# Optimization experiments

Measured on AMD Instinct MI355X. Metric: run time of the kernel, lower is better.

## Reference

```python
import jax, jax.numpy as jnp
import numpy as np

H = 32        # num_attention_heads
KVH = 8       # num_key_value_heads
D = 64        # head_dim
HID = 2048    # hidden_size
G = H // KVH  # num_key_value_groups


def setup_inputs() -> dict:
    key = jax.random.key(0)
    k1, k2, k3, k4, k5 = jax.random.split(key, 5)
    B, S = 1, 2048
    s = 1.0 / np.sqrt(HID)
    return {
        "hidden_states": jax.random.normal(k1, (B, S, HID), dtype=jnp.float32),
        "attention_mask": jnp.ones((B, S), dtype=jnp.int32),
        "Wq": jax.random.normal(k2, (H * D, HID), dtype=jnp.float32) * s,
        "Wk": jax.random.normal(k3, (KVH * D, HID), dtype=jnp.float32) * s,
        "Wv": jax.random.normal(k4, (KVH * D, HID), dtype=jnp.float32) * s,
        "Wo": jax.random.normal(k5, (HID, HID), dtype=jnp.float32) * s,
    }


def reference(hidden_states, attention_mask, Wq, Wk, Wv, Wo):
    B, S, _ = hidden_states.shape
    dtype = hidden_states.dtype

    q = (hidden_states @ Wq.T).reshape(B, S, H, D).transpose(0, 2, 1, 3)     # [B,H,S,D]
    k = (hidden_states @ Wk.T).reshape(B, S, KVH, D).transpose(0, 2, 1, 3)   # [B,KVH,S,D]
    v = (hidden_states @ Wv.T).reshape(B, S, KVH, D).transpose(0, 2, 1, 3)

    # repeat_interleave over head dim: each KV head serves G query heads
    k = jnp.repeat(k, G, axis=1)  # [B,H,S,D]
    v = jnp.repeat(v, G, axis=1)

    scores = jnp.einsum('bhqd,bhkd->bhqk', q, k) / np.sqrt(D)  # [B,H,S,S]

    causal = jnp.tril(jnp.ones((S, S), dtype=dtype))                # [S,S]
    am = attention_mask.astype(dtype)[:, None, None, :]              # [B,1,1,S]
    mask = am * causal[None, None, :, :]                             # [B,1,S,S]
    mask = (1.0 - mask) * jnp.finfo(dtype).min
    scores = scores + mask                                           # broadcast over heads

    weights = jax.nn.softmax(scores, axis=-1)
    attn = jnp.einsum('bhqk,bhkd->bhqd', weights, v)                 # [B,H,S,D]
    attn = attn.transpose(0, 2, 1, 3).reshape(B, S, HID)
    return attn @ Wo.T
```

## Files before the change

### kernel.cpp

```cpp
#include <hip/hip_runtime.h>
#include <hip/hip_bf16.h>
#include <math.h>

typedef __attribute__((ext_vector_type(4))) float f32x4;
typedef __attribute__((ext_vector_type(16))) float f32x16;
typedef __attribute__((ext_vector_type(8))) short bf16x8;
typedef __attribute__((ext_vector_type(4))) short s16x4;
typedef __attribute__((ext_vector_type(4))) unsigned int u32x4;
typedef __attribute__((ext_vector_type(2))) unsigned int u32x2;
typedef short s16;
typedef unsigned int u32;
typedef unsigned short u16;

#define S_LEN 2048
#define HIDN  2048
#define QKVW  3072
#define NH    32
#define NKVH  8
#define HD    64

__device__ __forceinline__ s16 f2bf(float f) {
  unsigned int u = __float_as_uint(f);
  unsigned int lsb = (u >> 16) & 1u;
  u += 0x7fffu + lsb;
  return (s16)(u >> 16);
}

__device__ __forceinline__ u32 cvtpk(float lo, float hi) {
  u32 r;
  asm("v_cvt_pk_bf16_f32 %0, %1, %2" : "=v"(r) : "v"(lo), "v"(hi));
  return r;
}

__device__ __forceinline__ void gload16(const void* g, void* l) {
  __builtin_amdgcn_global_load_lds(
      (const __attribute__((address_space(1))) void*)g,
      (__attribute__((address_space(3))) void*)l, 16, 0, 0);
}

__device__ __forceinline__ void pls(u32& a, u32& b) {
  asm volatile("v_permlane32_swap_b32 %0, %1" : "+v"(a), "+v"(b));
}

__device__ __forceinline__ int swz7(int row) { return (row ^ (row >> 3)) & 7; }

__global__ __launch_bounds__(256) void cvt_all(const float* __restrict__ h,
                                               const float* __restrict__ wq,
                                               const float* __restrict__ wk,
                                               const float* __restrict__ wv,
                                               const float* __restrict__ wo,
                                               s16x4* __restrict__ dst) {
  int i = blockIdx.x * 256 + threadIdx.x;
  const float* src; int off;
  if (i < 1048576)      { src = h;  off = i; }
  else if (i < 2097152) { src = wq; off = i - 1048576; }
  else if (i < 2359296) { src = wk; off = i - 2097152; }
  else if (i < 2621440) { src = wv; off = i - 2359296; }
  else                  { src = wo; off = i - 2621440; }
  if (i < 3670016) {
    float4 f = reinterpret_cast<const float4*>(src)[off];
    s16x4 o;
    o.x = f2bf(f.x); o.y = f2bf(f.y); o.z = f2bf(f.z); o.w = f2bf(f.w);
    dst[i] = o;
  }
}

__device__ __forceinline__ void storeC(s16* C, size_t idx, float v)   { C[idx] = f2bf(v); }
__device__ __forceinline__ void storeC(float* C, size_t idx, float v) { C[idx] = v; }

template <typename OUT_T>
__global__ __launch_bounds__(512) void gemm_bt(const s16* __restrict__ A,
                                               const s16* __restrict__ B,
                                               OUT_T* __restrict__ C,
                                               int M, int N, int K) {
  __shared__ alignas(16) s16 As[2][8192];
  __shared__ alignas(16) s16 Bs[2][8192];

  const int t    = threadIdx.x;
  const int lane = t & 63;
  const int w    = t >> 6;
  const int wr   = (w >> 2) * 64;
  const int wc   = (w & 3) * 32;
  const int lr   = lane & 15;
  const int lg   = lane >> 4;
  const int bm   = blockIdx.y * 128;
  const int bn   = blockIdx.x * 128;

  const int srow0 = (w * 2) * 8 + (lane >> 3);
  const int srow1 = (w * 2 + 1) * 8 + (lane >> 3);
  const int sl0   = ((lane & 7) ^ swz7(srow0)) * 8;
  const int sl1   = ((lane & 7) ^ swz7(srow1)) * 8;

  f32x4 acc[4][2];
#pragma unroll
  for (int m = 0; m < 4; ++m)
#pragma unroll
    for (int n = 0; n < 2; ++n)
      acc[m][n] = (f32x4){0.f, 0.f, 0.f, 0.f};

  const int nK = K >> 6;
  int buf = 0;

  {
    gload16(&A[(size_t)(bm + srow0) * K + sl0], (char*)As[0] + (w * 2) * 1024);
    gload16(&A[(size_t)(bm + srow1) * K + sl1], (char*)As[0] + (w * 2 + 1) * 1024);
    gload16(&B[(size_t)(bn + srow0) * K + sl0], (char*)Bs[0] + (w * 2) * 1024);
    gload16(&B[(size_t)(bn + srow1) * K + sl1], (char*)Bs[0] + (w * 2 + 1) * 1024);
  }
  __syncthreads();

  for (int ki = 0; ki < nK; ++ki) {
    if (ki + 1 < nK) {
      const int kt = (ki + 1) << 6;
      gload16(&A[(size_t)(bm + srow0) * K + kt + sl0], (char*)As[buf ^ 1] + (w * 2) * 1024);
      gload16(&A[(size_t)(bm + srow1) * K + kt + sl1], (char*)As[buf ^ 1] + (w * 2 + 1) * 1024);
      gload16(&B[(size_t)(bn + srow0) * K + kt + sl0], (char*)Bs[buf ^ 1] + (w * 2) * 1024);
      gload16(&B[(size_t)(bn + srow1) * K + kt + sl1], (char*)Bs[buf ^ 1] + (w * 2 + 1) * 1024);
    }

    bf16x8 af[4][2], bfr[2][2];
#pragma unroll
    for (int kk = 0; kk < 2; ++kk) {
#pragma unroll
      for (int m = 0; m < 4; ++m) {
        int row = wr + m * 16 + lr;
        af[m][kk] = *(bf16x8*)((char*)As[buf] + row * 128 + (((kk * 4 + lg) ^ swz7(row)) << 4));
      }
#pragma unroll
      for (int n = 0; n < 2; ++n) {
        int row = wc + n * 16 + lr;
        bfr[n][kk] = *(bf16x8*)((char*)Bs[buf] + row * 128 + (((kk * 4 + lg) ^ swz7(row)) << 4));
      }
    }

    __builtin_amdgcn_s_setprio(1);
#pragma unroll
    for (int m = 0; m < 4; ++m)
#pragma unroll
      for (int n = 0; n < 2; ++n)
#pragma unroll
        for (int kk = 0; kk < 2; ++kk)
          acc[m][n] = __builtin_amdgcn_mfma_f32_16x16x32_bf16(af[m][kk], bfr[n][kk], acc[m][n], 0, 0, 0);
    __builtin_amdgcn_s_setprio(0);

    __syncthreads();
    buf ^= 1;
  }

#pragma unroll
  for (int m = 0; m < 4; ++m)
#pragma unroll
    for (int n = 0; n < 2; ++n) {
      int row = bm + wr + m * 16 + lg * 4;
      int col = bn + wc + n * 16 + lr;
#pragma unroll
      for (int j = 0; j < 4; ++j)
        storeC(C, (size_t)(row + j) * N + col, acc[m][n][j]);
    }
}

__global__ __launch_bounds__(512) void attn_kernel(
    const s16* __restrict__ QKV,
    const int* __restrict__ am,
    s16* __restrict__ Ob) {
  __shared__ alignas(16) char smem[65536];
  __shared__ float2 mlb[4][64];

  const int t    = threadIdx.x;
  const int g    = t >> 8;
  const int tg   = t & 255;
  const int lane = t & 63;
  const int w    = tg >> 6;
  const int col  = lane & 31;
  const int hi   = lane >> 5;

  const int hk = blockIdx.x;
  const int qi = blockIdx.y;
  const int qt = (qi < 32) ? (63 - qi) : (qi - 32);
  const int h  = hk * 4 + w;
  const int nt = ((qt * 32 + 31) >> 6) + 1;
  const int R  = (nt + 1) >> 1;
  const int kbase = 2048 + hk * 64;
  const int vbase = 2560 + hk * 64;

  const float CF = 0.18033688f;

  const int krow   = lane >> 3;
  const int kslotb = lane & 7;
  const int vkv    = 2 * (tg >> 3);
  const int vd8    = (tg & 7) * 8;

  const int qrow = qt * 32 + col;
  bf16x8 qf[4];
#pragma unroll
  for (int ds = 0; ds < 4; ++ds)
    qf[ds] = *(const bf16x8*)&QKV[(size_t)qrow * QKVW + h * 64 + ds * 16 + hi * 8];

  if (g < nt) {
    char* Kn = smem + (g * 2 + 0) * 16384;
    char* Vn = Kn + 8192;
#pragma unroll
    for (int pp = 0; pp < 2; ++pp) {
      int c   = w * 2 + pp;
      int row = c * 8 + krow;
      int slot = kslotb ^ swz7(row);
      gload16(&QKV[(size_t)(g * 64 + row) * QKVW + kbase + slot * 8], Kn + c * 1024);
    }
    bf16x8 va = *(const bf16x8*)&QKV[(size_t)(g * 64 + vkv) * QKVW + vbase + vd8];
    bf16x8 vb = *(const bf16x8*)&QKV[(size_t)(g * 64 + vkv + 1) * QKVW + vbase + vd8];
#pragma unroll
    for (int i = 0; i < 8; ++i) {
      int d = vd8 + i;
      u32 pk = (u32)(u16)va[i] | ((u32)(u16)vb[i] << 16);
      *(u32*)&Vn[(d * 128 + vkv * 2) ^ (swz7(d) << 4)] = pk;
    }
  }
  int acur = am[g * 64 + lane];

  float m_i = -1e30f, l_part = 0.f;
  f32x16 Oacc[2];
#pragma unroll
  for (int b = 0; b < 2; ++b)
#pragma unroll
    for (int i = 0; i < 16; ++i) Oacc[b][i] = 0.f;
  __syncthreads();

  for (int it = 0; it < R; ++it) {
    const int buf  = it & 1;
    const int tile = 2 * it + g;
    const bool valid = (tile < nt);
    const int kv0  = tile * 64;
    const bool pre = (tile + 2 < nt);

    char* Kc = smem + (g * 2 + buf) * 16384;
    char* Vc = Kc + 8192;
    char* Kn = smem + (g * 2 + (buf ^ 1)) * 16384;
    char* Vn = Kn + 8192;

    bf16x8 va, vb;
    int anext = 0;
    if (pre) {
      const int nk0 = kv0 + 128;
#pragma unroll
      for (int pp = 0; pp < 2; ++pp) {
        int c   = w * 2 + pp;
        int row = c * 8 + krow;
        int slot = kslotb ^ swz7(row);
        gload16(&QKV[(size_t)(nk0 + row) * QKVW + kbase + slot * 8], Kn + c * 1024);
      }
      va = *(const bf16x8*)&QKV[(size_t)(nk0 + vkv) * QKVW + vbase + vd8];
      vb = *(const bf16x8*)&QKV[(size_t)(nk0 + vkv + 1) * QKVW + vbase + vd8];
      anext = am[nk0 + lane];
    }

    if (valid) {
      f32x16 s0, s1;
#pragma unroll
      for (int i = 0; i < 16; ++i) { s0[i] = 0.f; s1[i] = 0.f; }
      __builtin_amdgcn_s_setprio(1);
#pragma unroll
      for (int ds = 0; ds < 4; ++ds) {
        int off = ds * 32 + hi * 16;
        bf16x8 k0 = *(bf16x8*)&Kc[(col * 128 + off) ^ (swz7(col) << 4)];
        bf16x8 k1 = *(bf16x8*)&Kc[((32 + col) * 128 + off) ^ (swz7(32 + col) << 4)];
        s0 = __builtin_amdgcn_mfma_f32_32x32x16_bf16(k0, qf[ds], s0, 0, 0, 0);
        s1 = __builtin_amdgcn_mfma_f32_32x32x16_bf16(k1, qf[ds], s1, 0, 0, 0);
      }
      __builtin_amdgcn_s_setprio(0);

      float pvv[32];
      unsigned long long m64 = __ballot(acur != 0);
      bool interior = (kv0 + 64 <= qt * 32) && (m64 == ~0ull);
      if (interior) {
#pragma unroll
        for (int r = 0; r < 16; ++r) { pvv[r] = s0[r] * CF; pvv[16 + r] = s1[r] * CF; }
      } else {
#pragma unroll
        for (int b = 0; b < 2; ++b)
#pragma unroll
          for (int r = 0; r < 16; ++r) {
            int kvl = b * 32 + (r & 3) + 8 * (r >> 2) + 4 * hi;
            float sv = b ? s1[r] : s0[r];
            bool ok = (kv0 + kvl <= qrow) && ((m64 >> kvl) & 1ull);
            pvv[b * 16 + r] = ok ? sv * CF : -INFINITY;
          }
      }

      float a0 = pvv[0], a1 = pvv[1], a2 = pvv[2], a3 = pvv[3];
#pragma unroll
      for (int i = 4; i < 32; i += 4) {
        a0 = fmaxf(a0, pvv[i]);     a1 = fmaxf(a1, pvv[i + 1]);
        a2 = fmaxf(a2, pvv[i + 2]); a3 = fmaxf(a3, pvv[i + 3]);
      }
      float lmax = fmaxf(fmaxf(a0, a1), fmaxf(a2, a3));
      lmax = fmaxf(lmax, __shfl_xor(lmax, 32));

      if (!__all(lmax - m_i <= 8.f)) {
        float nm = fmaxf(m_i, lmax);
        float al = __builtin_amdgcn_exp2f(m_i - nm);
        m_i = nm;
        l_part *= al;
#pragma unroll
        for (int b = 0; b < 2; ++b)
#pragma unroll
          for (int i = 0; i < 16; ++i) Oacc[b][i] *= al;
      }

      float t0 = 0.f, t1 = 0.f, t2 = 0.f, t3 = 0.f;
#pragma unroll
      for (int i = 0; i < 32; i += 4) {
        pvv[i]     = __builtin_amdgcn_exp2f(pvv[i] - m_i);     t0 += pvv[i];
        pvv[i + 1] = __builtin_amdgcn_exp2f(pvv[i + 1] - m_i); t1 += pvv[i + 1];
        pvv[i + 2] = __builtin_amdgcn_exp2f(pvv[i + 2] - m_i); t2 += pvv[i + 2];
        pvv[i + 3] = __builtin_amdgcn_exp2f(pvv[i + 3] - m_i); t3 += pvv[i + 3];
      }
      l_part += (t0 + t1) + (t2 + t3);

      bf16x8 pf[4];
#pragma unroll
      for (int b = 0; b < 2; ++b)
#pragma unroll
        for (int gg = 0; gg < 2; ++gg) {
          int base = b * 16 + gg * 8;
          u32 A1 = cvtpk(pvv[base + 0], pvv[base + 1]);
          u32 A2 = cvtpk(pvv[base + 2], pvv[base + 3]);
          u32 B1 = cvtpk(pvv[base + 4], pvv[base + 5]);
          u32 B2 = cvtpk(pvv[base + 6], pvv[base + 7]);
          pls(A1, B1);
          pls(A2, B2);
          u32x4 pw; pw[0] = A1; pw[1] = A2; pw[2] = B1; pw[3] = B2;
          pf[b * 2 + gg] = *reinterpret_cast<bf16x8*>(&pw);
        }

      __builtin_amdgcn_s_setprio(1);
#pragma unroll
      for (int ks = 0; ks < 4; ++ks) {
        int off = ks * 32 + hi * 16;
#pragma unroll
        for (int db = 0; db < 2; ++db) {
          int d = db * 32 + col;
          bf16x8 vf = *(bf16x8*)&Vc[(d * 128 + off) ^ (swz7(d) << 4)];
          Oacc[db] = __builtin_amdgcn_mfma_f32_32x32x16_bf16(vf, pf[ks], Oacc[db], 0, 0, 0);
        }
      }
      __builtin_amdgcn_s_setprio(0);
    }

    if (pre) {
#pragma unroll
      for (int i = 0; i < 8; ++i) {
        int d = vd8 + i;
        u32 pk = (u32)(u16)va[i] | ((u32)(u16)vb[i] << 16);
        *(u32*)&Vn[(d * 128 + vkv * 2) ^ (swz7(d) << 4)] = pk;
      }
      acur = anext;
    }
    __syncthreads();
  }

  float l_p = l_part + __shfl_xor(l_part, 32);

  if (g == 0) {
    float* pool = (float*)smem + w * 2048 + lane * 32;
#pragma unroll
    for (int b = 0; b < 2; ++b)
#pragma unroll
      for (int i = 0; i < 16; ++i) pool[b * 16 + i] = Oacc[b][i];
    mlb[w][lane] = make_float2(m_i, l_p);
  }
  __syncthreads();
  if (g == 1) {
    const float* pool = (const float*)smem + w * 2048 + lane * 32;
    float2 ml0 = mlb[w][lane];
    float mm = fmaxf(ml0.x, m_i);
    float b0 = __builtin_amdgcn_exp2f(ml0.x - mm);
    float b1 = __builtin_amdgcn_exp2f(m_i - mm);
    float linv = 1.0f / (ml0.y * b0 + l_p * b1);
    float s0 = b0 * linv, s1v = b1 * linv;
#pragma unroll
    for (int db = 0; db < 2; ++db)
#pragma unroll
      for (int qd = 0; qd < 4; ++qd) {
        float o0 = pool[db * 16 + qd * 4 + 0] * s0 + Oacc[db][qd * 4 + 0] * s1v;
        float o1 = pool[db * 16 + qd * 4 + 1] * s0 + Oacc[db][qd * 4 + 1] * s1v;
        float o2 = pool[db * 16 + qd * 4 + 2] * s0 + Oacc[db][qd * 4 + 2] * s1v;
        float o3 = pool[db * 16 + qd * 4 + 3] * s0 + Oacc[db][qd * 4 + 3] * s1v;
        u32x2 o;
        o[0] = cvtpk(o0, o1);
        o[1] = cvtpk(o2, o3);
        int d0 = db * 32 + qd * 8 + hi * 4;
        *(u32x2*)&Ob[(size_t)qrow * HIDN + h * 64 + d0] = o;
      }
  }
}

extern "C" void kernel_launch(void* const* d_in, const int* in_sizes, int n_in,
                              void* d_out, int out_size, void* d_ws, size_t ws_size,
                              hipStream_t stream) {
  const float* hidden = (const float*)d_in[0];
  const int*   am     = (const int*)d_in[1];
  const float* Wq     = (const float*)d_in[2];
  const float* Wk     = (const float*)d_in[3];
  const float* Wv     = (const float*)d_in[4];
  const float* Wo     = (const float*)d_in[5];
  float* out = (float*)d_out;

  s16* hb    = (s16*)d_ws;
  s16* wqkvb = hb    + 4194304;
  s16* wob   = wqkvb + 6291456;
  s16* QKVb  = wob   + 4194304;
  s16* Ab    = QKVb  + 6291456;

  cvt_all<<<14336, 256, 0, stream>>>(hidden, Wq, Wk, Wv, Wo, (s16x4*)d_ws);

  gemm_bt<s16><<<dim3(24, 16), 512, 0, stream>>>(hb, wqkvb, QKVb, 2048, 3072, 2048);

  attn_kernel<<<dim3(8, 64), 512, 0, stream>>>(QKVb, am, Ab);

  gemm_bt<float><<<dim3(16, 16), 512, 0, stream>>>(Ab, wob, out, 2048, 2048, 2048);
}
```

Baseline: 140.7 us.

## Pair causal query tiles per attention block and split-K the output projection

The attention grid is halved so that each block processes two query tiles, a long one (63-p) and a short one (p), one after the other. This evens out the causal-mask workload across blocks. The softmax scale is now folded into an FMA inside the exp2 argument instead of a separate multiply per score. The output projection GEMM is split along K into two slices that accumulate with atomicAdd into a zeroed output, which doubles its grid to 512 blocks. The costs are a memset, atomic traffic on fp32 stores, and serialized phases inside each attention block.

```diff
diff --git a/kernel.cpp b/kernel.cpp
--- a/kernel.cpp
+++ b/kernel.cpp
@@ -65,14 +65,18 @@
   }
 }
 
-__device__ __forceinline__ void storeC(s16* C, size_t idx, float v)   { C[idx] = f2bf(v); }
-__device__ __forceinline__ void storeC(float* C, size_t idx, float v) { C[idx] = v; }
-
-template <typename OUT_T>
+template <bool ATOMIC>
+__device__ __forceinline__ void storeO(s16* C, size_t idx, float v)   { C[idx] = f2bf(v); }
+template <bool ATOMIC>
+__device__ __forceinline__ void storeO(float* C, size_t idx, float v) {
+  if (ATOMIC) atomicAdd(&C[idx], v); else C[idx] = v;
+}
+
+template <typename OUT_T, bool ATOMIC>
 __global__ __launch_bounds__(512) void gemm_bt(const s16* __restrict__ A,
                                                const s16* __restrict__ B,
                                                OUT_T* __restrict__ C,
-                                               int M, int N, int K) {
+                                               int M, int N, int ldk, int Kpart) {
   __shared__ alignas(16) s16 As[2][8192];
   __shared__ alignas(16) s16 Bs[2][8192];
 
@@ -86,6 +90,9 @@
   const int bm   = blockIdx.y * 128;
   const int bn   = blockIdx.x * 128;
 
+  A += (size_t)blockIdx.z * Kpart;
+  B += (size_t)blockIdx.z * Kpart;
+
   const int srow0 = (w * 2) * 8 + (lane >> 3);
   const int srow1 = (w * 2 + 1) * 8 + (lane >> 3);
   const int sl0   = ((lane & 7) ^ swz7(srow0)) * 8;
@@ -98,24 +105,24 @@
     for (int n = 0; n < 2; ++n)
       acc[m][n] = (f32x4){0.f, 0.f, 0.f, 0.f};
 
-  const int nK = K >> 6;
+  const int nK = Kpart >> 6;
   int buf = 0;
 
   {
-    gload16(&A[(size_t)(bm + srow0) * K + sl0], (char*)As[0] + (w * 2) * 1024);
-    gload16(&A[(size_t)(bm + srow1) * K + sl1], (char*)As[0] + (w * 2 + 1) * 1024);
-    gload16(&B[(size_t)(bn + srow0) * K + sl0], (char*)Bs[0] + (w * 2) * 1024);
-    gload16(&B[(size_t)(bn + srow1) * K + sl1], (char*)Bs[0] + (w * 2 + 1) * 1024);
+    gload16(&A[(size_t)(bm + srow0) * ldk + sl0], (char*)As[0] + (w * 2) * 1024);
+    gload16(&A[(size_t)(bm + srow1) * ldk + sl1], (char*)As[0] + (w * 2 + 1) * 1024);
+    gload16(&B[(size_t)(bn + srow0) * ldk + sl0], (char*)Bs[0] + (w * 2) * 1024);
+    gload16(&B[(size_t)(bn + srow1) * ldk + sl1], (char*)Bs[0] + (w * 2 + 1) * 1024);
   }
   __syncthreads();
 
   for (int ki = 0; ki < nK; ++ki) {
     if (ki + 1 < nK) {
       const int kt = (ki + 1) << 6;
-      gload16(&A[(size_t)(bm + srow0) * K + kt + sl0], (char*)As[buf ^ 1] + (w * 2) * 1024);
-      gload16(&A[(size_t)(bm + srow1) * K + kt + sl1], (char*)As[buf ^ 1] + (w * 2 + 1) * 1024);
-      gload16(&B[(size_t)(bn + srow0) * K + kt + sl0], (char*)Bs[buf ^ 1] + (w * 2) * 1024);
-      gload16(&B[(size_t)(bn + srow1) * K + kt + sl1], (char*)Bs[buf ^ 1] + (w * 2 + 1) * 1024);
+      gload16(&A[(size_t)(bm + srow0) * ldk + kt + sl0], (char*)As[buf ^ 1] + (w * 2) * 1024);
+      gload16(&A[(size_t)(bm + srow1) * ldk + kt + sl1], (char*)As[buf ^ 1] + (w * 2 + 1) * 1024);
+      gload16(&B[(size_t)(bn + srow0) * ldk + kt + sl0], (char*)Bs[buf ^ 1] + (w * 2) * 1024);
+      gload16(&B[(size_t)(bn + srow1) * ldk + kt + sl1], (char*)Bs[buf ^ 1] + (w * 2 + 1) * 1024);
     }
 
     bf16x8 af[4][2], bfr[2][2];
@@ -155,7 +162,7 @@
       int col = bn + wc + n * 16 + lr;
 #pragma unroll
       for (int j = 0; j < 4; ++j)
-        storeC(C, (size_t)(row + j) * N + col, acc[m][n][j]);
+        storeO<ATOMIC>(C, (size_t)(row + j) * N + col, acc[m][n][j]);
     }
 }
 
@@ -175,14 +182,10 @@
   const int hi   = lane >> 5;
 
   const int hk = blockIdx.x;
-  const int qi = blockIdx.y;
-  const int qt = (qi < 32) ? (63 - qi) : (qi - 32);
+  const int p  = blockIdx.y;
   const int h  = hk * 4 + w;
-  const int nt = ((qt * 32 + 31) >> 6) + 1;
-  const int R  = (nt + 1) >> 1;
   const int kbase = 2048 + hk * 64;
   const int vbase = 2560 + hk * 64;
-
   const float CF = 0.18033688f;
 
   const int krow   = lane >> 3;
@@ -190,207 +193,215 @@
   const int vkv    = 2 * (tg >> 3);
   const int vd8    = (tg & 7) * 8;
 
-  const int qrow = qt * 32 + col;
-  bf16x8 qf[4];
-#pragma unroll
-  for (int ds = 0; ds < 4; ++ds)
-    qf[ds] = *(const bf16x8*)&QKV[(size_t)qrow * QKVW + h * 64 + ds * 16 + hi * 8];
-
-  if (g < nt) {
-    char* Kn = smem + (g * 2 + 0) * 16384;
-    char* Vn = Kn + 8192;
-#pragma unroll
-    for (int pp = 0; pp < 2; ++pp) {
-      int c   = w * 2 + pp;
-      int row = c * 8 + krow;
-      int slot = kslotb ^ swz7(row);
-      gload16(&QKV[(size_t)(g * 64 + row) * QKVW + kbase + slot * 8], Kn + c * 1024);
-    }
-    bf16x8 va = *(const bf16x8*)&QKV[(size_t)(g * 64 + vkv) * QKVW + vbase + vd8];
-    bf16x8 vb = *(const bf16x8*)&QKV[(size_t)(g * 64 + vkv + 1) * QKVW + vbase + vd8];
-#pragma unroll
-    for (int i = 0; i < 8; ++i) {
-      int d = vd8 + i;
-      u32 pk = (u32)(u16)va[i] | ((u32)(u16)vb[i] << 16);
-      *(u32*)&Vn[(d * 128 + vkv * 2) ^ (swz7(d) << 4)] = pk;
-    }
-  }
-  int acur = am[g * 64 + lane];
-
-  float m_i = -1e30f, l_part = 0.f;
-  f32x16 Oacc[2];
-#pragma unroll
-  for (int b = 0; b < 2; ++b)
-#pragma unroll
-    for (int i = 0; i < 16; ++i) Oacc[b][i] = 0.f;
-  __syncthreads();
-
-  for (int it = 0; it < R; ++it) {
-    const int buf  = it & 1;
-    const int tile = 2 * it + g;
-    const bool valid = (tile < nt);
-    const int kv0  = tile * 64;
-    const bool pre = (tile + 2 < nt);
-
-    char* Kc = smem + (g * 2 + buf) * 16384;
-    char* Vc = Kc + 8192;
-    char* Kn = smem + (g * 2 + (buf ^ 1)) * 16384;
-    char* Vn = Kn + 8192;
-
-    bf16x8 va, vb;
-    int anext = 0;
-    if (pre) {
-      const int nk0 = kv0 + 128;
+  for (int phase = 0; phase < 2; ++phase) {
+    const int qt = phase ? p : 63 - p;
+    const int nt = (qt >> 1) + 1;
+    const int R  = (nt + 1) >> 1;
+    const int qrow = qt * 32 + col;
+
+    bf16x8 qf[4];
+#pragma unroll
+    for (int ds = 0; ds < 4; ++ds)
+      qf[ds] = *(const bf16x8*)&QKV[(size_t)qrow * QKVW + h * 64 + ds * 16 + hi * 8];
+
+    if (g < nt) {
+      char* Kn = smem + (g * 2 + 0) * 16384;
+      char* Vn = Kn + 8192;
 #pragma unroll
       for (int pp = 0; pp < 2; ++pp) {
         int c   = w * 2 + pp;
         int row = c * 8 + krow;
         int slot = kslotb ^ swz7(row);
-        gload16(&QKV[(size_t)(nk0 + row) * QKVW + kbase + slot * 8], Kn + c * 1024);
-      }
-      va = *(const bf16x8*)&QKV[(size_t)(nk0 + vkv) * QKVW + vbase + vd8];
-      vb = *(const bf16x8*)&QKV[(size_t)(nk0 + vkv + 1) * QKVW + vbase + vd8];
-      anext = am[nk0 + lane];
-    }
-
-    if (valid) {
-      f32x16 s0, s1;
-#pragma unroll
-      for (int i = 0; i < 16; ++i) { s0[i] = 0.f; s1[i] = 0.f; }
-      __builtin_amdgcn_s_setprio(1);
-#pragma unroll
-      for (int ds = 0; ds < 4; ++ds) {
-        int off = ds * 32 + hi * 16;
-        bf16x8 k0 = *(bf16x8*)&Kc[(col * 128 + off) ^ (swz7(col) << 4)];
-        bf16x8 k1 = *(bf16x8*)&Kc[((32 + col) * 128 + off) ^ (swz7(32 + col) << 4)];
-        s0 = __builtin_amdgcn_mfma_f32_32x32x16_bf16(k0, qf[ds], s0, 0, 0, 0);
-        s1 = __builtin_amdgcn_mfma_f32_32x32x16_bf16(k1, qf[ds], s1, 0, 0, 0);
-      }
-      __builtin_amdgcn_s_setprio(0);
-
-      float pvv[32];
-      unsigned long long m64 = __ballot(acur != 0);
-      bool interior = (kv0 + 64 <= qt * 32) && (m64 == ~0ull);
-      if (interior) {
-#pragma unroll
-        for (int r = 0; r < 16; ++r) { pvv[r] = s0[r] * CF; pvv[16 + r] = s1[r] * CF; }
-      } else {
-#pragma unroll
-        for (int b = 0; b < 2; ++b)
-#pragma unroll
-          for (int r = 0; r < 16; ++r) {
-            int kvl = b * 32 + (r & 3) + 8 * (r >> 2) + 4 * hi;
-            float sv = b ? s1[r] : s0[r];
-            bool ok = (kv0 + kvl <= qrow) && ((m64 >> kvl) & 1ull);
-            pvv[b * 16 + r] = ok ? sv * CF : -INFINITY;
-          }
-      }
-
-      float a0 = pvv[0], a1 = pvv[1], a2 = pvv[2], a3 = pvv[3];
-#pragma unroll
-      for (int i = 4; i < 32; i += 4) {
-        a0 = fmaxf(a0, pvv[i]);     a1 = fmaxf(a1, pvv[i + 1]);
-        a2 = fmaxf(a2, pvv[i + 2]); a3 = fmaxf(a3, pvv[i + 3]);
-      }
-      float lmax = fmaxf(fmaxf(a0, a1), fmaxf(a2, a3));
-      lmax = fmaxf(lmax, __shfl_xor(lmax, 32));
-
-      if (!__all(lmax - m_i <= 8.f)) {
-        float nm = fmaxf(m_i, lmax);
-        float al = __builtin_amdgcn_exp2f(m_i - nm);
-        m_i = nm;
-        l_part *= al;
-#pragma unroll
-        for (int b = 0; b < 2; ++b)
-#pragma unroll
-          for (int i = 0; i < 16; ++i) Oacc[b][i] *= al;
-      }
-
-      float t0 = 0.f, t1 = 0.f, t2 = 0.f, t3 = 0.f;
-#pragma unroll
-      for (int i = 0; i < 32; i += 4) {
-        pvv[i]     = __builtin_amdgcn_exp2f(pvv[i] - m_i);     t0 += pvv[i];
-        pvv[i + 1] = __builtin_amdgcn_exp2f(pvv[i + 1] - m_i); t1 += pvv[i + 1];
-        pvv[i + 2] = __builtin_amdgcn_exp2f(pvv[i + 2] - m_i); t2 += pvv[i + 2];
-        pvv[i + 3] = __builtin_amdgcn_exp2f(pvv[i + 3] - m_i); t3 += pvv[i + 3];
-      }
-      l_part += (t0 + t1) + (t2 + t3);
-
-      bf16x8 pf[4];
-#pragma unroll
-      for (int b = 0; b < 2; ++b)
-#pragma unroll
-        for (int gg = 0; gg < 2; ++gg) {
-          int base = b * 16 + gg * 8;
-          u32 A1 = cvtpk(pvv[base + 0], pvv[base + 1]);
-          u32 A2 = cvtpk(pvv[base + 2], pvv[base + 3]);
-          u32 B1 = cvtpk(pvv[base + 4], pvv[base + 5]);
-          u32 B2 = cvtpk(pvv[base + 6], pvv[base + 7]);
-          pls(A1, B1);
-          pls(A2, B2);
-          u32x4 pw; pw[0] = A1; pw[1] = A2; pw[2] = B1; pw[3] = B2;
-          pf[b * 2 + gg] = *reinterpret_cast<bf16x8*>(&pw);
-        }
-
-      __builtin_amdgcn_s_setprio(1);
-#pragma unroll
-      for (int ks = 0; ks < 4; ++ks) {
-        int off = ks * 32 + hi * 16;
-#pragma unroll
-        for (int db = 0; db < 2; ++db) {
-          int d = db * 32 + col;
-          bf16x8 vf = *(bf16x8*)&Vc[(d * 128 + off) ^ (swz7(d) << 4)];
-          Oacc[db] = __builtin_amdgcn_mfma_f32_32x32x16_bf16(vf, pf[ks], Oacc[db], 0, 0, 0);
-        }
-      }
-      __builtin_amdgcn_s_setprio(0);
-    }
-
-    if (pre) {
+        gload16(&QKV[(size_t)(g * 64 + row) * QKVW + kbase + slot * 8], Kn + c * 1024);
+      }
+      bf16x8 va = *(const bf16x8*)&QKV[(size_t)(g * 64 + vkv) * QKVW + vbase + vd8];
+      bf16x8 vb = *(const bf16x8*)&QKV[(size_t)(g * 64 + vkv + 1) * QKVW + vbase + vd8];
 #pragma unroll
       for (int i = 0; i < 8; ++i) {
         int d = vd8 + i;
         u32 pk = (u32)(u16)va[i] | ((u32)(u16)vb[i] << 16);
         *(u32*)&Vn[(d * 128 + vkv * 2) ^ (swz7(d) << 4)] = pk;
       }
-      acur = anext;
-    }
+    }
+    int acur = am[g * 64 + lane];
+
+    float m_i = -1e30f, l_part = 0.f;
+    f32x16 Oacc[2];
+#pragma unroll
+    for (int b = 0; b < 2; ++b)
+#pragma unroll
+      for (int i = 0; i < 16; ++i) Oacc[b][i] = 0.f;
     __syncthreads();
-  }
-
-  float l_p = l_part + __shfl_xor(l_part, 32);
-
-  if (g == 0) {
-    float* pool = (float*)smem + w * 2048 + lane * 32;
-#pragma unroll
-    for (int b = 0; b < 2; ++b)
-#pragma unroll
-      for (int i = 0; i < 16; ++i) pool[b * 16 + i] = Oacc[b][i];
-    mlb[w][lane] = make_float2(m_i, l_p);
-  }
-  __syncthreads();
-  if (g == 1) {
-    const float* pool = (const float*)smem + w * 2048 + lane * 32;
-    float2 ml0 = mlb[w][lane];
-    float mm = fmaxf(ml0.x, m_i);
-    float b0 = __builtin_amdgcn_exp2f(ml0.x - mm);
-    float b1 = __builtin_amdgcn_exp2f(m_i - mm);
-    float linv = 1.0f / (ml0.y * b0 + l_p * b1);
-    float s0 = b0 * linv, s1v = b1 * linv;
-#pragma unroll
-    for (int db = 0; db < 2; ++db)
-#pragma unroll
-      for (int qd = 0; qd < 4; ++qd) {
-        float o0 = pool[db * 16 + qd * 4 + 0] * s0 + Oacc[db][qd * 4 + 0] * s1v;
-        float o1 = pool[db * 16 + qd * 4 + 1] * s0 + Oacc[db][qd * 4 + 1] * s1v;
-        float o2 = pool[db * 16 + qd * 4 + 2] * s0 + Oacc[db][qd * 4 + 2] * s1v;
-        float o3 = pool[db * 16 + qd * 4 + 3] * s0 + Oacc[db][qd * 4 + 3] * s1v;
-        u32x2 o;
-        o[0] = cvtpk(o0, o1);
-        o[1] = cvtpk(o2, o3);
-        int d0 = db * 32 + qd * 8 + hi * 4;
-        *(u32x2*)&Ob[(size_t)qrow * HIDN + h * 64 + d0] = o;
-      }
+
+    for (int it = 0; it < R; ++it) {
+      const int buf  = it & 1;
+      const int tile = 2 * it + g;
+      const bool valid = (tile < nt);
+      const int kv0  = tile * 64;
+      const bool pre = (tile + 2 < nt);
+
+      char* Kc = smem + (g * 2 + buf) * 16384;
+      char* Vc = Kc + 8192;
+      char* Kn = smem + (g * 2 + (buf ^ 1)) * 16384;
+      char* Vn = Kn + 8192;
+
+      bf16x8 va, vb;
+      int anext = 0;
+      if (pre) {
+        const int nk0 = kv0 + 128;
+#pragma unroll
+        for (int pp = 0; pp < 2; ++pp) {
+          int c   = w * 2 + pp;
+          int row = c * 8 + krow;
+          int slot = kslotb ^ swz7(row);
+          gload16(&QKV[(size_t)(nk0 + row) * QKVW + kbase + slot * 8], Kn + c * 1024);
+        }
+        va = *(const bf16x8*)&QKV[(size_t)(nk0 + vkv) * QKVW + vbase + vd8];
+        vb = *(const bf16x8*)&QKV[(size_t)(nk0 + vkv + 1) * QKVW + vbase + vd8];
+        anext = am[nk0 + lane];
+      }
+
+      if (valid) {
+        f32x16 s0, s1;
+#pragma unroll
+        for (int i = 0; i < 16; ++i) { s0[i] = 0.f; s1[i] = 0.f; }
+        __builtin_amdgcn_s_setprio(1);
+#pragma unroll
+        for (int ds = 0; ds < 4; ++ds) {
+          int off = ds * 32 + hi * 16;
+          bf16x8 k0 = *(bf16x8*)&Kc[(col * 128 + off) ^ (swz7(col) << 4)];
+          bf16x8 k1 = *(bf16x8*)&Kc[((32 + col) * 128 + off) ^ (swz7(32 + col) << 4)];
+          s0 = __builtin_amdgcn_mfma_f32_32x32x16_bf16(k0, qf[ds], s0, 0, 0, 0);
+          s1 = __builtin_amdgcn_mfma_f32_32x32x16_bf16(k1, qf[ds], s1, 0, 0, 0);
+        }
+        __builtin_amdgcn_s_setprio(0);
+
+        float pvv[32];
+        unsigned long long m64 = __ballot(acur != 0);
+        bool interior = (kv0 + 64 <= qt * 32) && (m64 == ~0ull);
+        if (interior) {
+#pragma unroll
+          for (int r = 0; r < 16; ++r) { pvv[r] = s0[r]; pvv[16 + r] = s1[r]; }
+        } else {
+#pragma unroll
+          for (int b = 0; b < 2; ++b)
+#pragma unroll
+            for (int r = 0; r < 16; ++r) {
+              int kvl = b * 32 + (r & 3) + 8 * (r >> 2) + 4 * hi;
+              float sv = b ? s1[r] : s0[r];
+              bool ok = (kv0 + kvl <= qrow) && ((m64 >> kvl) & 1ull);
+              pvv[b * 16 + r] = ok ? sv : -INFINITY;
+            }
+        }
+
+        float a0 = pvv[0], a1 = pvv[1], a2 = pvv[2], a3 = pvv[3];
+#pragma unroll
+        for (int i = 4; i < 32; i += 4) {
+          a0 = fmaxf(a0, pvv[i]);     a1 = fmaxf(a1, pvv[i + 1]);
+          a2 = fmaxf(a2, pvv[i + 2]); a3 = fmaxf(a3, pvv[i + 3]);
+        }
+        float lmax = fmaxf(fmaxf(a0, a1), fmaxf(a2, a3));
+        lmax = fmaxf(lmax, __shfl_xor(lmax, 32));
+        float lmaxs = lmax * CF;
+
+        if (!__all(lmaxs - m_i <= 8.f)) {
+          float nm = fmaxf(m_i, lmaxs);
+          float al = __builtin_amdgcn_exp2f(m_i - nm);
+          m_i = nm;
+          l_part *= al;
+#pragma unroll
+          for (int b = 0; b < 2; ++b)
+#pragma unroll
+            for (int i = 0; i < 16; ++i) Oacc[b][i] *= al;
+        }
+
+        float t0 = 0.f, t1 = 0.f, t2 = 0.f, t3 = 0.f;
+#pragma unroll
+        for (int i = 0; i < 32; i += 4) {
+          pvv[i]     = __builtin_amdgcn_exp2f(__builtin_fmaf(pvv[i],     CF, -m_i)); t0 += pvv[i];
+          pvv[i + 1] = __builtin_amdgcn_exp2f(__builtin_fmaf(pvv[i + 1], CF, -m_i)); t1 += pvv[i + 1];
+          pvv[i + 2] = __builtin_amdgcn_exp2f(__builtin_fmaf(pvv[i + 2], CF, -m_i)); t2 += pvv[i + 2];
+          pvv[i + 3] = __builtin_amdgcn_exp2f(__builtin_fmaf(pvv[i + 3], CF, -m_i)); t3 += pvv[i + 3];
+        }
+        l_part += (t0 + t1) + (t2 + t3);
+
+        bf16x8 pf[4];
+#pragma unroll
+        for (int b = 0; b < 2; ++b)
+#pragma unroll
+          for (int gg = 0; gg < 2; ++gg) {
+            int base = b * 16 + gg * 8;
+            u32 A1 = cvtpk(pvv[base + 0], pvv[base + 1]);
+            u32 A2 = cvtpk(pvv[base + 2], pvv[base + 3]);
+            u32 B1 = cvtpk(pvv[base + 4], pvv[base + 5]);
+            u32 B2 = cvtpk(pvv[base + 6], pvv[base + 7]);
+            pls(A1, B1);
+            pls(A2, B2);
+            u32x4 pw; pw[0] = A1; pw[1] = A2; pw[2] = B1; pw[3] = B2;
+            pf[b * 2 + gg] = *reinterpret_cast<bf16x8*>(&pw);
+          }
+
+        __builtin_amdgcn_s_setprio(1);
+#pragma unroll
+        for (int ks = 0; ks < 4; ++ks) {
+          int off = ks * 32 + hi * 16;
+#pragma unroll
+          for (int db = 0; db < 2; ++db) {
+            int d = db * 32 + col;
+            bf16x8 vf = *(bf16x8*)&Vc[(d * 128 + off) ^ (swz7(d) << 4)];
+            Oacc[db] = __builtin_amdgcn_mfma_f32_32x32x16_bf16(vf, pf[ks], Oacc[db], 0, 0, 0);
+          }
+        }
+        __builtin_amdgcn_s_setprio(0);
+      }
+
+      if (pre) {
+#pragma unroll
+        for (int i = 0; i < 8; ++i) {
+          int d = vd8 + i;
+          u32 pk = (u32)(u16)va[i] | ((u32)(u16)vb[i] << 16);
+          *(u32*)&Vn[(d * 128 + vkv * 2) ^ (swz7(d) << 4)] = pk;
+        }
+        acur = anext;
+      }
+      __syncthreads();
+    }
+
+    float l_p = l_part + __shfl_xor(l_part, 32);
+
+    if (g == 0) {
+      float* pool = (float*)smem + w * 2048 + lane * 32;
+#pragma unroll
+      for (int b = 0; b < 2; ++b)
+#pragma unroll
+        for (int i = 0; i < 16; ++i) pool[b * 16 + i] = Oacc[b][i];
+      mlb[w][lane] = make_float2(m_i, l_p);
+    }
+    __syncthreads();
+    if (g == 1) {
+      const float* pool = (const float*)smem + w * 2048 + lane * 32;
+      float2 ml0 = mlb[w][lane];
+      float mm = fmaxf(ml0.x, m_i);
+      float b0 = __builtin_amdgcn_exp2f(ml0.x - mm);
+      float b1 = __builtin_amdgcn_exp2f(m_i - mm);
+      float linv = 1.0f / (ml0.y * b0 + l_p * b1);
+      float sc0 = b0 * linv, sc1 = b1 * linv;
+#pragma unroll
+      for (int db = 0; db < 2; ++db)
+#pragma unroll
+        for (int qd = 0; qd < 4; ++qd) {
+          float o0 = pool[db * 16 + qd * 4 + 0] * sc0 + Oacc[db][qd * 4 + 0] * sc1;
+          float o1 = pool[db * 16 + qd * 4 + 1] * sc0 + Oacc[db][qd * 4 + 1] * sc1;
+          float o2 = pool[db * 16 + qd * 4 + 2] * sc0 + Oacc[db][qd * 4 + 2] * sc1;
+          float o3 = pool[db * 16 + qd * 4 + 3] * sc0 + Oacc[db][qd * 4 + 3] * sc1;
+          u32x2 o;
+          o[0] = cvtpk(o0, o1);
+          o[1] = cvtpk(o2, o3);
+          int d0 = db * 32 + qd * 8 + hi * 4;
+          *(u32x2*)&Ob[(size_t)qrow * HIDN + h * 64 + d0] = o;
+        }
+    }
+    __syncthreads();
   }
 }
 
@@ -413,9 +424,10 @@
 
   cvt_all<<<14336, 256, 0, stream>>>(hidden, Wq, Wk, Wv, Wo, (s16x4*)d_ws);
 
-  gemm_bt<s16><<<dim3(24, 16), 512, 0, stream>>>(hb, wqkvb, QKVb, 2048, 3072, 2048);
-
-  attn_kernel<<<dim3(8, 64), 512, 0, stream>>>(QKVb, am, Ab);
-
-  gemm_bt<float><<<dim3(16, 16), 512, 0, stream>>>(Ab, wob, out, 2048, 2048, 2048);
-}
+  gemm_bt<s16, false><<<dim3(24, 16, 1), 512, 0, stream>>>(hb, wqkvb, QKVb, 2048, 3072, 2048, 2048);
+
+  attn_kernel<<<dim3(8, 32), 512, 0, stream>>>(QKVb, am, Ab);
+
+  hipMemsetAsync(d_out, 0, (size_t)out_size * sizeof(float), stream);
+  gemm_bt<float, true><<<dim3(16, 16, 2), 512, 0, stream>>>(Ab, wob, out, 2048, 2048, 2048, 1024);
+}
```

Measured after the change: 143.6 us. +2.1%, slower.
